# Performance work log

Hardware: AMD Instinct MI355X
Metric: run time of the kernel (lower is better)

Reference implementation:

```python
import jax, jax.numpy as jnp
import numpy as np

TAU_PRE = 2.0
TAU_POST = 2.0


def setup_inputs() -> dict:
    key = jax.random.key(0)
    k1, k2, k3 = jax.random.split(key, 3)
    T, B, PRE, POST = 64, 16, 4096, 4096
    in_spikes = jax.random.uniform(k1, (T, B, PRE), dtype=jnp.float32)
    out_spikes = jax.random.uniform(k2, (T, B, POST), dtype=jnp.float32)
    weight = jax.random.normal(k3, (POST, PRE), dtype=jnp.float32)
    return {"in_spikes": in_spikes, "out_spikes": out_spikes, "weight": weight}


def reference(in_spikes, out_spikes, weight):
    # in_spikes: [T, B, pre]; out_spikes: [T, B, post]; weight: [post, pre]
    T, B, PRE = in_spikes.shape
    POST = out_spikes.shape[-1]

    def step(carry, xs):
        trace_pre, trace_post, delta_w = carry
        i_sp, o_sp = xs
        trace_pre = jnp.clip(trace_pre - trace_pre / TAU_PRE + i_sp, 0.0, 1.0)  # [B, pre]
        trace_post = trace_post - trace_post / TAU_POST + o_sp  # [B, post]
        # sum_b o[b,post]*trace_pre[b,pre] - (sum_b o[b,post]*trace_post[b,post]) * w[post,pre]
        dw = (jnp.einsum('bo,bp->op', o_sp, trace_pre)
              - (o_sp * trace_post).sum(0)[:, None] * weight)
        return (trace_pre, trace_post, delta_w + dw), None

    init = (jnp.zeros((B, PRE), in_spikes.dtype),
            jnp.zeros((B, POST), out_spikes.dtype),
            jnp.zeros((POST, PRE), weight.dtype))
    (trace_pre, trace_post, delta_w), _ = jax.lax.scan(step, init, (in_spikes, out_spikes))
    return delta_w
```

## Files before the change

kernel.cpp:

```cpp
#include <hip/hip_runtime.h>


#define T_STEPS 64
#define B_SZ    16
#define PRE     4096
#define POST    4096
#define K_TOT   1024

typedef __attribute__((ext_vector_type(8))) unsigned short ushort8;
typedef __attribute__((ext_vector_type(8))) __bf16 bf16x8;
typedef __attribute__((ext_vector_type(4))) float floatx4;

__device__ __forceinline__ unsigned short f2bf(float f) {
    unsigned int u = __float_as_uint(f);
    u += 0x7fff + ((u >> 16) & 1);
    return (unsigned short)(u >> 16);
}

__global__ __launch_bounds__(256) void trace_convert(
        const float* __restrict__ in_spikes,
        const float* __restrict__ out_spikes,
        unsigned short* __restrict__ AT,
        unsigned short* __restrict__ BT,
        float* __restrict__ coef) {
    __shared__ unsigned short tile[16][K_TOT];
    __shared__ float cbuf[16][17];
    const int tid = threadIdx.x;
    const int b  = tid >> 4;
    const int xl = tid & 15;
    const bool isA = blockIdx.x >= 256;
    const int x0 = (isA ? blockIdx.x - 256 : blockIdx.x) * 16;
    const float* src = (isA ? out_spikes : in_spikes) + (size_t)b * 4096 + x0 + xl;
    unsigned short* dst = isA ? AT : BT;

    float state = 0.f, c = 0.f;
    for (int tc = 0; tc < 4; ++tc) {
        float xs[16];
        #pragma unroll
        for (int j = 0; j < 16; ++j)
            xs[j] = src[(size_t)(tc * 16 + j) * (B_SZ * PRE)];
        if (isA) {
            #pragma unroll
            for (int j = 0; j < 16; ++j) {
                const int t = tc * 16 + j;
                state = 0.5f * state + xs[j];
                c += xs[j] * state;
                tile[xl][(t * 16 + b + xl * 8) & (K_TOT - 1)] = f2bf(xs[j]);
            }
        } else {
            #pragma unroll
            for (int j = 0; j < 16; ++j) {
                const int t = tc * 16 + j;
                state = fminf(fmaxf(0.5f * state + xs[j], 0.f), 1.f);
                tile[xl][(t * 16 + b + xl * 8) & (K_TOT - 1)] = f2bf(state);
            }
        }
    }
    if (isA) cbuf[b][xl] = c;
    __syncthreads();
    if (isA && tid < 16) {
        float s = 0.f;
        #pragma unroll
        for (int bb = 0; bb < 16; ++bb) s += cbuf[bb][tid];
        coef[x0 + tid] = s;
    }
    const int row = tid >> 4;
    const int c0  = tid & 15;
    #pragma unroll
    for (int i = 0; i < 8; ++i) {
        const int ch = c0 + i * 16;
        ushort8 v = *(const ushort8*)&tile[row][((ch + row) & 127) * 8];
        *(ushort8*)&dst[(size_t)(x0 + row) * K_TOT + ch * 8] = v;
    }
}

#define BM 128
#define BN 128
#define BK 32

__device__ __forceinline__ void glds16(const void* g, void* l) {
    __builtin_amdgcn_global_load_lds((const __attribute__((address_space(1))) void*)g,
                                     (__attribute__((address_space(3))) void*)l,
                                     16, 0, 0);
}

__global__ __launch_bounds__(256) void stdp_gemm_mfma(
        const unsigned short* __restrict__ AT,
        const unsigned short* __restrict__ BT,
        const float* __restrict__ W,
        const float* __restrict__ coef,
        float* __restrict__ Cout) {
    __shared__ unsigned short As[BM][BK];
    __shared__ unsigned short Bs[BN][BK];
    const int tid  = threadIdx.x;
    const int lane = tid & 63;
    const int wave = tid >> 6;
    const int wm = (wave >> 1) * 64;
    const int wn = (wave & 1) * 64;
    const int m0 = blockIdx.y * BM;
    const int n0 = blockIdx.x * BN;

    floatx4 acc[4][4];
    #pragma unroll
    for (int i = 0; i < 4; ++i)
        #pragma unroll
        for (int j = 0; j < 4; ++j)
            acc[i][j] = (floatx4){0.f, 0.f, 0.f, 0.f};

    const int srow = tid >> 2;
    const int qg   = (tid & 3) ^ ((srow >> 1) & 3);
    const unsigned short* ga = &AT[(size_t)(m0 + srow) * K_TOT + qg * 8];
    const unsigned short* gb = &BT[(size_t)(n0 + srow) * K_TOT + qg * 8];
    unsigned short* la = &As[0][0] + wave * 512;
    unsigned short* lb = &Bs[0][0] + wave * 512;

    const int rm  = lane & 15;
    const int q   = lane >> 4;
    const int kqs = (q ^ ((rm >> 1) & 3)) * 8;

    for (int k0 = 0; k0 < K_TOT; k0 += BK) {
        glds16(ga,              la);
        glds16(ga + 64 * K_TOT, la + 64 * BK);
        glds16(gb,              lb);
        glds16(gb + 64 * K_TOT, lb + 64 * BK);
        ga += BK; gb += BK;
        __syncthreads();

        bf16x8 af[4], bv[4];
        #pragma unroll
        for (int i = 0; i < 4; ++i) {
            af[i] = *(const bf16x8*)&As[wm + i * 16 + rm][kqs];
            bv[i] = *(const bf16x8*)&Bs[wn + i * 16 + rm][kqs];
        }
        #pragma unroll
        for (int mi = 0; mi < 4; ++mi)
            #pragma unroll
            for (int ni = 0; ni < 4; ++ni)
                acc[mi][ni] = __builtin_amdgcn_mfma_f32_16x16x32_bf16(
                    af[mi], bv[ni], acc[mi][ni], 0, 0, 0);
        __syncthreads();
    }

    const int colp = n0 + wn + rm;
    const int rowb = m0 + wm + (lane >> 4) * 4;
    #pragma unroll
    for (int mi = 0; mi < 4; ++mi) {
        #pragma unroll
        for (int r = 0; r < 4; ++r) {
            const int o = rowb + mi * 16 + r;
            const float cf = coef[o];
            const float* wr = &W[(size_t)o * PRE];
            float* cr = &Cout[(size_t)o * PRE];
            #pragma unroll
            for (int ni = 0; ni < 4; ++ni) {
                const int p = colp + ni * 16;
                cr[p] = acc[mi][ni][r] - cf * wr[p];
            }
        }
    }
}

extern "C" void kernel_launch(void* const* d_in, const int* in_sizes, int n_in,
                              void* d_out, int out_size, void* d_ws, size_t ws_size,
                              hipStream_t stream) {
    const float* in_spikes  = (const float*)d_in[0];
    const float* out_spikes = (const float*)d_in[1];
    const float* weight     = (const float*)d_in[2];
    float* out = (float*)d_out;

    unsigned short* AT = (unsigned short*)d_ws;
    unsigned short* BT = AT + (size_t)POST * K_TOT;
    float* coef = (float*)(BT + (size_t)PRE * K_TOT);

    trace_convert<<<512, 256, 0, stream>>>(in_spikes, out_spikes, AT, BT, coef);

    dim3 grid(PRE / BN, POST / BM);
    stdp_gemm_mfma<<<grid, 256, 0, stream>>>(AT, BT, weight, coef, out);
}
```

Baseline: 191.3 us.

## Stage trace_convert inputs through LDS with async global_load_lds in time chunks

Rewrites the trace/convert prepass so each block handles 32 features and stages 8-timestep chunks of spikes into LDS via global_load_lds 16-byte loads. The old version used scattered strided per-thread scalar loads. It then transposes into a padded bf16 tile and writes K-contiguous rows chunk by chunk. The grid shrinks from 512 to 256 blocks. This is meant to improve load coalescing and memory-level parallelism for the prepass, at the cost of fewer blocks and extra barriers per chunk.

```diff
diff --git a/kernel.cpp b/kernel.cpp
--- a/kernel.cpp
+++ b/kernel.cpp
@@ -17,72 +17,92 @@
     return (unsigned short)(u >> 16);
 }
 
+__device__ __forceinline__ void glds16(const void* g, void* l) {
+    __builtin_amdgcn_global_load_lds((const __attribute__((address_space(1))) void*)g,
+                                     (__attribute__((address_space(3))) void*)l,
+                                     16, 0, 0);
+}
+
 __global__ __launch_bounds__(256) void trace_convert(
         const float* __restrict__ in_spikes,
         const float* __restrict__ out_spikes,
         unsigned short* __restrict__ AT,
         unsigned short* __restrict__ BT,
         float* __restrict__ coef) {
-    __shared__ unsigned short tile[16][K_TOT];
-    __shared__ float cbuf[16][17];
-    const int tid = threadIdx.x;
-    const int b  = tid >> 4;
-    const int xl = tid & 15;
-    const bool isA = blockIdx.x >= 256;
-    const int x0 = (isA ? blockIdx.x - 256 : blockIdx.x) * 16;
-    const float* src = (isA ? out_spikes : in_spikes) + (size_t)b * 4096 + x0 + xl;
+    __shared__ float ldsf[4096];
+    __shared__ unsigned short ot[128 * 34];
+    __shared__ float cbuf[8][33];
+    const int tid  = threadIdx.x;
+    const int wave = tid >> 6;
+    const int lane = tid & 63;
+    const bool isA = blockIdx.x >= 128;
+    const int p0 = (blockIdx.x & 127) * 32;
+    const float* src = isA ? out_spikes : in_spikes;
     unsigned short* dst = isA ? AT : BT;
 
-    float state = 0.f, c = 0.f;
-    for (int tc = 0; tc < 4; ++tc) {
-        float xs[16];
+    const int bA = tid >> 5;
+    const int pA = tid & 31;
+
+    float st0 = 0.f, st1 = 0.f, c0 = 0.f, c1 = 0.f;
+
+    for (int tc = 0; tc < 8; ++tc) {
+        const int T0 = tc * 8;
         #pragma unroll
-        for (int j = 0; j < 16; ++j)
-            xs[j] = src[(size_t)(tc * 16 + j) * (B_SZ * PRE)];
-        if (isA) {
-            #pragma unroll
-            for (int j = 0; j < 16; ++j) {
-                const int t = tc * 16 + j;
-                state = 0.5f * state + xs[j];
-                c += xs[j] * state;
-                tile[xl][(t * 16 + b + xl * 8) & (K_TOT - 1)] = f2bf(xs[j]);
-            }
-        } else {
-            #pragma unroll
-            for (int j = 0; j < 16; ++j) {
-                const int t = tc * 16 + j;
-                state = fminf(fmaxf(0.5f * state + xs[j], 0.f), 1.f);
-                tile[xl][(t * 16 + b + xl * 8) & (K_TOT - 1)] = f2bf(state);
+        for (int i = 0; i < 4; ++i) {
+            const int q  = (wave * 4 + i) * 64 + lane;
+            const int p  = (q & 7) * 4;
+            const int b  = (q >> 3) & 15;
+            const int tl = q >> 7;
+            const float* g = src + ((size_t)((T0 + tl) * 16 + b)) * 4096 + p0 + p;
+            glds16(g, (char*)ldsf + (size_t)(wave * 4 + i) * 1024);
+        }
+        __syncthreads();
+
+        #pragma unroll
+        for (int tl = 0; tl < 8; ++tl) {
+            const float x0 = ldsf[tl * 512 + bA * 32 + pA];
+            const float x1 = ldsf[tl * 512 + (bA + 8) * 32 + pA];
+            if (isA) {
+                st0 = 0.5f * st0 + x0; c0 += x0 * st0;
+                st1 = 0.5f * st1 + x1; c1 += x1 * st1;
+                ot[(tl * 16 + bA)     * 34 + pA] = f2bf(x0);
+                ot[(tl * 16 + bA + 8) * 34 + pA] = f2bf(x1);
+            } else {
+                st0 = fminf(fmaxf(0.5f * st0 + x0, 0.f), 1.f);
+                st1 = fminf(fmaxf(0.5f * st1 + x1, 0.f), 1.f);
+                ot[(tl * 16 + bA)     * 34 + pA] = f2bf(st0);
+                ot[(tl * 16 + bA + 8) * 34 + pA] = f2bf(st1);
             }
         }
+        __syncthreads();
+
+        const int pf = tid >> 3;
+        const int c8 = tid & 7;
+        #pragma unroll
+        for (int i = 0; i < 2; ++i) {
+            const int ch = c8 + i * 8;
+            ushort8 v;
+            #pragma unroll
+            for (int s = 0; s < 8; ++s) v[s] = ot[(ch * 8 + s) * 34 + pf];
+            *(ushort8*)&dst[(size_t)(p0 + pf) * K_TOT + T0 * 16 + ch * 8] = v;
+        }
     }
-    if (isA) cbuf[b][xl] = c;
-    __syncthreads();
-    if (isA && tid < 16) {
-        float s = 0.f;
-        #pragma unroll
-        for (int bb = 0; bb < 16; ++bb) s += cbuf[bb][tid];
-        coef[x0 + tid] = s;
-    }
-    const int row = tid >> 4;
-    const int c0  = tid & 15;
-    #pragma unroll
-    for (int i = 0; i < 8; ++i) {
-        const int ch = c0 + i * 16;
-        ushort8 v = *(const ushort8*)&tile[row][((ch + row) & 127) * 8];
-        *(ushort8*)&dst[(size_t)(x0 + row) * K_TOT + ch * 8] = v;
+
+    if (isA) {
+        cbuf[bA][pA] = c0 + c1;
+        __syncthreads();
+        if (tid < 32) {
+            float s = 0.f;
+            #pragma unroll
+            for (int r = 0; r < 8; ++r) s += cbuf[r][tid];
+            coef[p0 + tid] = s;
+        }
     }
 }
 
 #define BM 128
 #define BN 128
 #define BK 32
-
-__device__ __forceinline__ void glds16(const void* g, void* l) {
-    __builtin_amdgcn_global_load_lds((const __attribute__((address_space(1))) void*)g,
-                                     (__attribute__((address_space(3))) void*)l,
-                                     16, 0, 0);
-}
 
 __global__ __launch_bounds__(256) void stdp_gemm_mfma(
         const unsigned short* __restrict__ AT,
@@ -172,7 +192,7 @@
     unsigned short* BT = AT + (size_t)POST * K_TOT;
     float* coef = (float*)(BT + (size_t)PRE * K_TOT);
 
-    trace_convert<<<512, 256, 0, stream>>>(in_spikes, out_spikes, AT, BT, coef);
+    trace_convert<<<256, 256, 0, stream>>>(in_spikes, out_spikes, AT, BT, coef);
 
     dim3 grid(PRE / BN, POST / BM);
     stdp_gemm_mfma<<<grid, 256, 0, stream>>>(AT, BT, weight, coef, out);
```

After: 191.6 us. About the same (+0.1%).
